# Kernel optimization log

Measured on AMD Instinct MI355X. Metric: run time of the kernel, lower is better.

## Reference

```python
import jax, jax.numpy as jnp
import numpy as np
import math

THETA = 2.0 ** 16  # rope theta from module (2**16)


def _freqs(n, theta):
    # get_freqs: quantize(arange(n), q=2) -> floor(i/2)*2; freqs = 1/theta**(q/n)/(2*pi)
    i = jnp.arange(n, dtype=jnp.float32)
    q = jnp.floor(i / 2.0) * 2.0
    return 1.0 / (theta ** (q / n)) / (2.0 * math.pi)


def _rope(phases, v):
    # interleaved rotation: v_rot = stack((-v[...,1::2], v[...,::2]), -1).reshape(v.shape)
    v_rot = jnp.stack((-v[..., 1::2], v[..., ::2]), axis=-1).reshape(v.shape)
    ph = (phases % 1.0) * (2.0 * math.pi)
    return v * jnp.cos(ph) + v_rot * jnp.sin(ph)


def setup_inputs() -> dict:
    key = jax.random.key(0)
    k1, k2, k3 = jax.random.split(key, 3)
    B, H, T, N = 2, 12, 2048, 256
    Q = jax.random.normal(k1, (B, H, T, N), dtype=jnp.float32)
    K = jax.random.normal(k2, (B, H, T, N), dtype=jnp.float32)
    V = jax.random.normal(k3, (B, H, T, N), dtype=jnp.float32)
    return {"Q": Q, "K": K, "V": V}


def reference(Q, K, V):
    T, N = Q.shape[2], Q.shape[3]
    freqs = _freqs(N, THETA)                                    # [N]
    phases = jnp.arange(T, dtype=jnp.float32)[:, None] * freqs  # [T, N]
    QR = _rope(phases, Q)
    KR = _rope(phases, K)
    # strictly-causal (diagonal=-1) non-softmax linear attention
    scores = jnp.einsum('bhtn,bhsn->bhts', QR, KR)
    scores = jnp.tril(scores, k=-1)
    return jnp.einsum('bhts,bhsn->bhtn', scores, V)
```

## Files before the change

### kernel.cpp

```cpp
#include <hip/hip_runtime.h>

typedef __bf16 bf16_t;
typedef short s16x8 __attribute__((ext_vector_type(8)));
typedef __bf16 bf16x4 __attribute__((ext_vector_type(4)));
typedef float f32x4 __attribute__((ext_vector_type(4)));

#define BH   24
#define TT   2048
#define NN   256

__global__ __launch_bounds__(256) void rope_qk_kernel(
    const float* __restrict__ Q, const float* __restrict__ K,
    bf16_t* __restrict__ QR, bf16_t* __restrict__ KR)
{
    int gid = blockIdx.x * 256 + threadIdx.x;
    int idx = gid * 8;
    int n0 = idx & (NN - 1);
    int t  = (idx >> 8) & (TT - 1);

    float4 q0 = *(const float4*)(Q + idx);
    float4 q1 = *(const float4*)(Q + idx + 4);
    float4 k0 = *(const float4*)(K + idx);
    float4 k1 = *(const float4*)(K + idx + 4);
    float qv[8] = {q0.x, q0.y, q0.z, q0.w, q1.x, q1.y, q1.z, q1.w};
    float kv[8] = {k0.x, k0.y, k0.z, k0.w, k1.x, k1.y, k1.z, k1.w};

    bf16_t qo[8], ko[8];
    #pragma unroll
    for (int j = 0; j < 4; j++) {
        int n = n0 + 2 * j;
        float freq = exp2f(-(float)n * 0.0625f) * 0.15915494309189535f;
        float ph = (float)t * freq;
        float r = ph - floorf(ph);
        float s = __builtin_amdgcn_sinf(r);
        float c = __builtin_amdgcn_cosf(r);
        qo[2*j]   = (bf16_t)(qv[2*j] * c - qv[2*j+1] * s);
        qo[2*j+1] = (bf16_t)(qv[2*j+1] * c + qv[2*j] * s);
        ko[2*j]   = (bf16_t)(kv[2*j] * c - kv[2*j+1] * s);
        ko[2*j+1] = (bf16_t)(kv[2*j+1] * c + kv[2*j] * s);
    }
    *(s16x8*)(QR + idx) = *(s16x8*)qo;
    *(s16x8*)(KR + idx) = *(s16x8*)ko;
}

__global__ __launch_bounds__(256) void vtrans_kernel(
    const float* __restrict__ V, bf16_t* __restrict__ Vt)
{
    __shared__ bf16_t tile[64][68];
    int bh = blockIdx.z;
    int t0 = blockIdx.x * 64;
    int n0 = blockIdx.y * 64;
    int rr = threadIdx.x >> 4;
    int c4 = (threadIdx.x & 15) * 4;

    const float* vb = V + ((long)bh * TT + t0) * NN + n0;
    #pragma unroll
    for (int i = 0; i < 4; i++) {
        int row = rr + i * 16;
        float4 v = *(const float4*)(vb + (long)row * NN + c4);
        bf16x4 b;
        b[0] = (bf16_t)v.x; b[1] = (bf16_t)v.y; b[2] = (bf16_t)v.z; b[3] = (bf16_t)v.w;
        *(bf16x4*)&tile[row][c4] = b;
    }
    __syncthreads();
    bf16_t* ob = Vt + ((long)bh * NN + n0) * TT + t0;
    #pragma unroll
    for (int i = 0; i < 4; i++) {
        int n = rr + i * 16;
        bf16x4 b;
        b[0] = tile[c4 + 0][n]; b[1] = tile[c4 + 1][n];
        b[2] = tile[c4 + 2][n]; b[3] = tile[c4 + 3][n];
        *(bf16x4*)(ob + (long)n * TT + c4) = b;
    }
}

__global__ __launch_bounds__(256, 2) void attn_kernel(
    const bf16_t* __restrict__ QR, const bf16_t* __restrict__ KR,
    const bf16_t* __restrict__ Vt, float* __restrict__ Out)
{
    __shared__ bf16_t kr_s[32][256];
    __shared__ bf16_t vt_s[256][40];
    __shared__ bf16_t s_s[4][32][40];

    int bh   = blockIdx.y;
    int qt   = 15 - (int)blockIdx.x;
    int t0   = qt * 128;
    int tid  = threadIdx.x;
    int wave = tid >> 6;
    int lane = tid & 63;
    int lrow = lane & 15;
    int lhi  = lane >> 4;
    int trow_base = t0 + wave * 32;

    s16x8 qfrag[2][8];
    #pragma unroll
    for (int rt = 0; rt < 2; rt++) {
        const bf16_t* qb = QR + ((long)bh * TT + trow_base + rt * 16 + lrow) * NN + lhi * 8;
        #pragma unroll
        for (int kb = 0; kb < 8; kb++)
            qfrag[rt][kb] = *(const s16x8*)(qb + kb * 32);
    }

    f32x4 zero4 = {0.0f, 0.0f, 0.0f, 0.0f};
    f32x4 oacc[2][16];
    #pragma unroll
    for (int rt = 0; rt < 2; rt++)
        #pragma unroll
        for (int nt = 0; nt < 16; nt++) oacc[rt][nt] = zero4;

    int krow  = tid >> 3;
    int kcolb = (tid & 7) * 64;
    const bf16_t* krbase = KR + ((long)bh * TT + krow) * NN + (tid & 7) * 32;
    const bf16_t* vtbase = Vt + ((long)bh * NN + tid) * TT;

    int ns = (t0 + 128) >> 5;
    for (int st = 0; st < ns; st++) {
        int s0 = st << 5;

        {
            const bf16_t* src = krbase + (long)s0 * NN;
            char* dst = (char*)(&kr_s[0][0]) + krow * 512;
            #pragma unroll
            for (int c = 0; c < 4; c++) {
                s16x8 v = *(const s16x8*)(src + c * 8);
                *(s16x8*)(dst + ((kcolb + c * 16) ^ ((krow & 7) << 4))) = v;
            }
        }
        {
            const bf16_t* src = vtbase + s0;
            #pragma unroll
            for (int c = 0; c < 4; c++)
                *(s16x8*)(&vt_s[tid][c * 8]) = *(const s16x8*)(src + c * 8);
        }
        __syncthreads();

        if (s0 < trow_base + 32) {
            f32x4 sacc[2][2];
            sacc[0][0] = zero4; sacc[0][1] = zero4; sacc[1][0] = zero4; sacc[1][1] = zero4;
            #pragma unroll
            for (int kb = 0; kb < 8; kb++) {
                #pragma unroll
                for (int h2 = 0; h2 < 2; h2++) {
                    int srow = h2 * 16 + lrow;
                    s16x8 bfr = *(const s16x8*)((char*)(&kr_s[0][0]) + srow * 512 +
                                    ((kb * 64 + lhi * 16) ^ ((srow & 7) << 4)));
                    sacc[0][h2] = __builtin_amdgcn_mfma_f32_16x16x32_bf16(
                                      qfrag[0][kb], bfr, sacc[0][h2], 0, 0, 0);
                    sacc[1][h2] = __builtin_amdgcn_mfma_f32_16x16x32_bf16(
                                      qfrag[1][kb], bfr, sacc[1][h2], 0, 0, 0);
                }
            }
            #pragma unroll
            for (int rt = 0; rt < 2; rt++)
                #pragma unroll
                for (int h2 = 0; h2 < 2; h2++)
                    #pragma unroll
                    for (int r = 0; r < 4; r++) {
                        int t_g = trow_base + rt * 16 + lhi * 4 + r;
                        int s_g = s0 + h2 * 16 + lrow;
                        float v = (s_g < t_g) ? sacc[rt][h2][r] : 0.0f;
                        s_s[wave][rt * 16 + lhi * 4 + r][h2 * 16 + lrow] = (bf16_t)v;
                    }
            s16x8 afr0 = *(const s16x8*)(&s_s[wave][lrow][lhi * 8]);
            s16x8 afr1 = *(const s16x8*)(&s_s[wave][16 + lrow][lhi * 8]);
            #pragma unroll
            for (int nt = 0; nt < 16; nt++) {
                s16x8 bfr = *(const s16x8*)(&vt_s[nt * 16 + lrow][lhi * 8]);
                oacc[0][nt] = __builtin_amdgcn_mfma_f32_16x16x32_bf16(afr0, bfr, oacc[0][nt], 0, 0, 0);
                oacc[1][nt] = __builtin_amdgcn_mfma_f32_16x16x32_bf16(afr1, bfr, oacc[1][nt], 0, 0, 0);
            }
        }
        __syncthreads();
    }

    #pragma unroll
    for (int rt = 0; rt < 2; rt++) {
        float* ob = Out + ((long)bh * TT + trow_base + rt * 16 + lhi * 4) * NN + lrow;
        #pragma unroll
        for (int nt = 0; nt < 16; nt++)
            #pragma unroll
            for (int r = 0; r < 4; r++)
                ob[(long)r * NN + nt * 16] = oacc[rt][nt][r];
    }
}

extern "C" void kernel_launch(void* const* d_in, const int* in_sizes, int n_in,
                              void* d_out, int out_size, void* d_ws, size_t ws_size,
                              hipStream_t stream) {
    const float* Q = (const float*)d_in[0];
    const float* K = (const float*)d_in[1];
    const float* V = (const float*)d_in[2];
    float* Out = (float*)d_out;

    const long TOT = (long)BH * TT * NN;
    bf16_t* qr = (bf16_t*)d_ws;
    bf16_t* kr = qr + TOT;
    bf16_t* vt = kr + TOT;

    rope_qk_kernel<<<dim3((int)(TOT / 8 / 256)), dim3(256), 0, stream>>>(Q, K, qr, kr);
    vtrans_kernel<<<dim3(TT / 64, NN / 64, BH), dim3(256), 0, stream>>>(V, vt);
    attn_kernel<<<dim3(TT / 128, BH), dim3(256), 0, stream>>>(qr, kr, vt, Out);
}
```

Measured before the change: 406.5 us.

## Split attention into 64-row tiles with split-K atomics for balanced causal work

```diff
diff --git a/kernel.cpp b/kernel.cpp
--- a/kernel.cpp
+++ b/kernel.cpp
@@ -8,6 +8,15 @@
 #define BH   24
 #define TT   2048
 #define NN   256
+
+__global__ __launch_bounds__(256) void zero_upper_kernel(float* __restrict__ Out)
+{
+    int gid = blockIdx.x * 256 + threadIdx.x;
+    int bh  = gid >> 16;
+    int off = gid & 65535;
+    float4* p = (float4*)(Out + (long)bh * (TT * NN) + 1024 * NN);
+    p[off] = make_float4(0.f, 0.f, 0.f, 0.f);
+}
 
 __global__ __launch_bounds__(256) void rope_qk_kernel(
     const float* __restrict__ Q, const float* __restrict__ K,
@@ -74,113 +83,122 @@
     }
 }
 
-__global__ __launch_bounds__(256, 2) void attn_kernel(
+__global__ __launch_bounds__(256, 3) void attn_kernel(
     const bf16_t* __restrict__ QR, const bf16_t* __restrict__ KR,
     const bf16_t* __restrict__ Vt, float* __restrict__ Out)
 {
-    __shared__ bf16_t kr_s[32][256];
+    __shared__ bf16_t kr_s[32 * 256];
     __shared__ bf16_t vt_s[256][40];
-    __shared__ bf16_t s_s[4][32][40];
-
-    int bh   = blockIdx.y;
-    int qt   = 15 - (int)blockIdx.x;
-    int t0   = qt * 128;
+    __shared__ bf16_t s_s[4][16][40];
+
+    int bh = blockIdx.y;
+    int x  = blockIdx.x;
+    int qt    = (x < 16) ? (16 + x) : (47 - x);
+    int chunk = (x >= 16 && x < 32) ? 1 : 0;
+    bool doAtomic = (qt >= 16);
+    int t0 = qt * 64;
+
     int tid  = threadIdx.x;
     int wave = tid >> 6;
     int lane = tid & 63;
     int lrow = lane & 15;
     int lhi  = lane >> 4;
-    int trow_base = t0 + wave * 32;
-
-    s16x8 qfrag[2][8];
-    #pragma unroll
-    for (int rt = 0; rt < 2; rt++) {
-        const bf16_t* qb = QR + ((long)bh * TT + trow_base + rt * 16 + lrow) * NN + lhi * 8;
+    int trow = t0 + wave * 16;
+
+    s16x8 qfrag[8];
+    {
+        const bf16_t* qb = QR + ((long)bh * TT + trow + lrow) * NN + lhi * 8;
         #pragma unroll
         for (int kb = 0; kb < 8; kb++)
-            qfrag[rt][kb] = *(const s16x8*)(qb + kb * 32);
-    }
-
-    f32x4 zero4 = {0.0f, 0.0f, 0.0f, 0.0f};
-    f32x4 oacc[2][16];
-    #pragma unroll
-    for (int rt = 0; rt < 2; rt++)
-        #pragma unroll
-        for (int nt = 0; nt < 16; nt++) oacc[rt][nt] = zero4;
-
-    int krow  = tid >> 3;
-    int kcolb = (tid & 7) * 64;
-    const bf16_t* krbase = KR + ((long)bh * TT + krow) * NN + (tid & 7) * 32;
-    const bf16_t* vtbase = Vt + ((long)bh * NN + tid) * TT;
-
-    int ns = (t0 + 128) >> 5;
-    for (int st = 0; st < ns; st++) {
+            qfrag[kb] = *(const s16x8*)(qb + kb * 32);
+    }
+
+    f32x4 zero4 = {0.f, 0.f, 0.f, 0.f};
+    f32x4 oacc[16];
+    #pragma unroll
+    for (int nt = 0; nt < 16; nt++) oacc[nt] = zero4;
+
+    int krow = tid >> 3;
+    int kch  = tid & 7;
+    const bf16_t* krsrc = KR + ((long)bh * TT + krow) * NN + kch * 32;
+    char* krdst = (char*)kr_s + krow * 512 + ((kch << 4) ^ ((krow & 7) << 4));
+    const bf16_t* vtsrc = Vt + ((long)bh * NN + tid) * TT;
+
+    int s_lo = chunk ? 1024 : 0;
+    int s_hi = chunk ? (t0 + 64) : min(t0 + 64, 1024);
+    int st0 = s_lo >> 5, st1 = s_hi >> 5;
+
+    for (int st = st0; st < st1; st++) {
         int s0 = st << 5;
 
         {
-            const bf16_t* src = krbase + (long)s0 * NN;
-            char* dst = (char*)(&kr_s[0][0]) + krow * 512;
-            #pragma unroll
-            for (int c = 0; c < 4; c++) {
-                s16x8 v = *(const s16x8*)(src + c * 8);
-                *(s16x8*)(dst + ((kcolb + c * 16) ^ ((krow & 7) << 4))) = v;
-            }
+            const bf16_t* src = krsrc + (long)s0 * NN;
+            #pragma unroll
+            for (int i = 0; i < 4; i++)
+                *(s16x8*)(krdst + i * 128) = *(const s16x8*)(src + i * 8);
         }
         {
-            const bf16_t* src = vtbase + s0;
+            const bf16_t* src = vtsrc + s0;
             #pragma unroll
             for (int c = 0; c < 4; c++)
                 *(s16x8*)(&vt_s[tid][c * 8]) = *(const s16x8*)(src + c * 8);
         }
         __syncthreads();
 
-        if (s0 < trow_base + 32) {
-            f32x4 sacc[2][2];
-            sacc[0][0] = zero4; sacc[0][1] = zero4; sacc[1][0] = zero4; sacc[1][1] = zero4;
+        if (s0 < trow + 16) {
+            f32x4 sacc[2];
+            sacc[0] = zero4; sacc[1] = zero4;
             #pragma unroll
             for (int kb = 0; kb < 8; kb++) {
                 #pragma unroll
                 for (int h2 = 0; h2 < 2; h2++) {
                     int srow = h2 * 16 + lrow;
-                    s16x8 bfr = *(const s16x8*)((char*)(&kr_s[0][0]) + srow * 512 +
-                                    ((kb * 64 + lhi * 16) ^ ((srow & 7) << 4)));
-                    sacc[0][h2] = __builtin_amdgcn_mfma_f32_16x16x32_bf16(
-                                      qfrag[0][kb], bfr, sacc[0][h2], 0, 0, 0);
-                    sacc[1][h2] = __builtin_amdgcn_mfma_f32_16x16x32_bf16(
-                                      qfrag[1][kb], bfr, sacc[1][h2], 0, 0, 0);
+                    s16x8 bfr = *(const s16x8*)((char*)kr_s + srow * 512 + lhi * 128 +
+                                    ((kb << 4) ^ ((srow & 7) << 4)));
+                    sacc[h2] = __builtin_amdgcn_mfma_f32_16x16x32_bf16(
+                                   qfrag[kb], bfr, sacc[h2], 0, 0, 0);
                 }
             }
-            #pragma unroll
-            for (int rt = 0; rt < 2; rt++)
+            if (s0 + 32 > trow) {
                 #pragma unroll
                 for (int h2 = 0; h2 < 2; h2++)
                     #pragma unroll
                     for (int r = 0; r < 4; r++) {
-                        int t_g = trow_base + rt * 16 + lhi * 4 + r;
+                        int t_g = trow + lhi * 4 + r;
                         int s_g = s0 + h2 * 16 + lrow;
-                        float v = (s_g < t_g) ? sacc[rt][h2][r] : 0.0f;
-                        s_s[wave][rt * 16 + lhi * 4 + r][h2 * 16 + lrow] = (bf16_t)v;
+                        float v = (s_g < t_g) ? sacc[h2][r] : 0.0f;
+                        s_s[wave][lhi * 4 + r][h2 * 16 + lrow] = (bf16_t)v;
                     }
-            s16x8 afr0 = *(const s16x8*)(&s_s[wave][lrow][lhi * 8]);
-            s16x8 afr1 = *(const s16x8*)(&s_s[wave][16 + lrow][lhi * 8]);
+            } else {
+                #pragma unroll
+                for (int h2 = 0; h2 < 2; h2++)
+                    #pragma unroll
+                    for (int r = 0; r < 4; r++)
+                        s_s[wave][lhi * 4 + r][h2 * 16 + lrow] = (bf16_t)sacc[h2][r];
+            }
+            s16x8 afr = *(const s16x8*)(&s_s[wave][lrow][lhi * 8]);
             #pragma unroll
             for (int nt = 0; nt < 16; nt++) {
                 s16x8 bfr = *(const s16x8*)(&vt_s[nt * 16 + lrow][lhi * 8]);
-                oacc[0][nt] = __builtin_amdgcn_mfma_f32_16x16x32_bf16(afr0, bfr, oacc[0][nt], 0, 0, 0);
-                oacc[1][nt] = __builtin_amdgcn_mfma_f32_16x16x32_bf16(afr1, bfr, oacc[1][nt], 0, 0, 0);
+                oacc[nt] = __builtin_amdgcn_mfma_f32_16x16x32_bf16(afr, bfr, oacc[nt], 0, 0, 0);
             }
         }
         __syncthreads();
     }
 
-    #pragma unroll
-    for (int rt = 0; rt < 2; rt++) {
-        float* ob = Out + ((long)bh * TT + trow_base + rt * 16 + lhi * 4) * NN + lrow;
+    float* ob = Out + ((long)bh * TT + trow + lhi * 4) * NN + lrow;
+    if (doAtomic) {
         #pragma unroll
         for (int nt = 0; nt < 16; nt++)
             #pragma unroll
             for (int r = 0; r < 4; r++)
-                ob[(long)r * NN + nt * 16] = oacc[rt][nt][r];
+                atomicAdd(&ob[(long)r * NN + nt * 16], oacc[nt][r]);
+    } else {
+        #pragma unroll
+        for (int nt = 0; nt < 16; nt++)
+            #pragma unroll
+            for (int r = 0; r < 4; r++)
+                ob[(long)r * NN + nt * 16] = oacc[nt][r];
     }
 }
 
@@ -197,7 +215,8 @@
     bf16_t* kr = qr + TOT;
     bf16_t* vt = kr + TOT;
 
+    zero_upper_kernel<<<dim3(BH * 256), dim3(256), 0, stream>>>(Out);
     rope_qk_kernel<<<dim3((int)(TOT / 8 / 256)), dim3(256), 0, stream>>>(Q, K, qr, kr);
     vtrans_kernel<<<dim3(TT / 64, NN / 64, BH), dim3(256), 0, stream>>>(V, vt);
-    attn_kernel<<<dim3(TT / 128, BH), dim3(256), 0, stream>>>(qr, kr, vt, Out);
-}
+    attn_kernel<<<dim3(48, BH), dim3(256), 0, stream>>>(qr, kr, vt, Out);
+}
```

Result: faster. 352.4 us (-13.3%).

## Switch causal attention to chunked linear-attention state formulation

Applied to the files above, without the earlier changes.

```diff
diff --git a/kernel.cpp b/kernel.cpp
--- a/kernel.cpp
+++ b/kernel.cpp
@@ -5,182 +5,229 @@
 typedef __bf16 bf16x4 __attribute__((ext_vector_type(4)));
 typedef float f32x4 __attribute__((ext_vector_type(4)));
 
-#define BH   24
-#define TT   2048
-#define NN   256
-
-__global__ __launch_bounds__(256) void rope_qk_kernel(
-    const float* __restrict__ Q, const float* __restrict__ K,
-    bf16_t* __restrict__ QR, bf16_t* __restrict__ KR)
-{
-    int gid = blockIdx.x * 256 + threadIdx.x;
-    int idx = gid * 8;
-    int n0 = idx & (NN - 1);
-    int t  = (idx >> 8) & (TT - 1);
-
-    float4 q0 = *(const float4*)(Q + idx);
-    float4 q1 = *(const float4*)(Q + idx + 4);
-    float4 k0 = *(const float4*)(K + idx);
-    float4 k1 = *(const float4*)(K + idx + 4);
-    float qv[8] = {q0.x, q0.y, q0.z, q0.w, q1.x, q1.y, q1.z, q1.w};
-    float kv[8] = {k0.x, k0.y, k0.z, k0.w, k1.x, k1.y, k1.z, k1.w};
-
-    bf16_t qo[8], ko[8];
-    #pragma unroll
-    for (int j = 0; j < 4; j++) {
-        int n = n0 + 2 * j;
-        float freq = exp2f(-(float)n * 0.0625f) * 0.15915494309189535f;
-        float ph = (float)t * freq;
-        float r = ph - floorf(ph);
-        float s = __builtin_amdgcn_sinf(r);
-        float c = __builtin_amdgcn_cosf(r);
-        qo[2*j]   = (bf16_t)(qv[2*j] * c - qv[2*j+1] * s);
-        qo[2*j+1] = (bf16_t)(qv[2*j+1] * c + qv[2*j] * s);
-        ko[2*j]   = (bf16_t)(kv[2*j] * c - kv[2*j+1] * s);
-        ko[2*j+1] = (bf16_t)(kv[2*j+1] * c + kv[2*j] * s);
-    }
-    *(s16x8*)(QR + idx) = *(s16x8*)qo;
-    *(s16x8*)(KR + idx) = *(s16x8*)ko;
-}
-
-__global__ __launch_bounds__(256) void vtrans_kernel(
-    const float* __restrict__ V, bf16_t* __restrict__ Vt)
+#define BH 24
+#define TT 2048
+#define NN 256
+
+__global__ __launch_bounds__(256) void rope_trans_kernel(
+    const float* __restrict__ src, bf16_t* __restrict__ dstRow,
+    bf16_t* __restrict__ dstT, int doRope)
 {
     __shared__ bf16_t tile[64][68];
-    int bh = blockIdx.z;
-    int t0 = blockIdx.x * 64;
-    int n0 = blockIdx.y * 64;
-    int rr = threadIdx.x >> 4;
-    int c4 = (threadIdx.x & 15) * 4;
-
-    const float* vb = V + ((long)bh * TT + t0) * NN + n0;
+    int bh = blockIdx.z, t0 = blockIdx.x * 64, n0 = blockIdx.y * 64;
+    int rr = threadIdx.x >> 4, c4 = (threadIdx.x & 15) * 4;
     #pragma unroll
     for (int i = 0; i < 4; i++) {
         int row = rr + i * 16;
-        float4 v = *(const float4*)(vb + (long)row * NN + c4);
+        int t = t0 + row;
+        float4 v = *(const float4*)(src + ((long)bh * TT + t) * NN + n0 + c4);
         bf16x4 b;
-        b[0] = (bf16_t)v.x; b[1] = (bf16_t)v.y; b[2] = (bf16_t)v.z; b[3] = (bf16_t)v.w;
+        if (doRope) {
+            float f0 = exp2f(-(float)(n0 + c4) * 0.0625f) * 0.15915494309189535f;
+            float f1 = exp2f(-(float)(n0 + c4 + 2) * 0.0625f) * 0.15915494309189535f;
+            float p0 = (float)t * f0; p0 -= floorf(p0);
+            float p1 = (float)t * f1; p1 -= floorf(p1);
+            float s0 = __builtin_amdgcn_sinf(p0), c0 = __builtin_amdgcn_cosf(p0);
+            float s1 = __builtin_amdgcn_sinf(p1), c1 = __builtin_amdgcn_cosf(p1);
+            b[0] = (bf16_t)(v.x * c0 - v.y * s0);
+            b[1] = (bf16_t)(v.y * c0 + v.x * s0);
+            b[2] = (bf16_t)(v.z * c1 - v.w * s1);
+            b[3] = (bf16_t)(v.w * c1 + v.z * s1);
+        } else {
+            b[0] = (bf16_t)v.x; b[1] = (bf16_t)v.y; b[2] = (bf16_t)v.z; b[3] = (bf16_t)v.w;
+        }
         *(bf16x4*)&tile[row][c4] = b;
-    }
-    __syncthreads();
-    bf16_t* ob = Vt + ((long)bh * NN + n0) * TT + t0;
-    #pragma unroll
-    for (int i = 0; i < 4; i++) {
-        int n = rr + i * 16;
-        bf16x4 b;
-        b[0] = tile[c4 + 0][n]; b[1] = tile[c4 + 1][n];
-        b[2] = tile[c4 + 2][n]; b[3] = tile[c4 + 3][n];
-        *(bf16x4*)(ob + (long)n * TT + c4) = b;
+        if (dstRow) *(bf16x4*)(dstRow + ((long)bh * TT + t) * NN + n0 + c4) = b;
+    }
+    if (dstT) {
+        __syncthreads();
+        #pragma unroll
+        for (int i = 0; i < 4; i++) {
+            int n = rr + i * 16;
+            bf16x4 b;
+            b[0] = tile[c4][n]; b[1] = tile[c4 + 1][n];
+            b[2] = tile[c4 + 2][n]; b[3] = tile[c4 + 3][n];
+            *(bf16x4*)(dstT + ((long)bh * NN + n0 + n) * TT + t0 + c4) = b;
+        }
     }
 }
 
 __global__ __launch_bounds__(256, 2) void attn_kernel(
     const bf16_t* __restrict__ QR, const bf16_t* __restrict__ KR,
-    const bf16_t* __restrict__ Vt, float* __restrict__ Out)
+    const bf16_t* __restrict__ KRt, const bf16_t* __restrict__ Vt,
+    float* __restrict__ Out)
 {
-    __shared__ bf16_t kr_s[32][256];
-    __shared__ bf16_t vt_s[256][40];
-    __shared__ bf16_t s_s[4][32][40];
-
-    int bh   = blockIdx.y;
-    int qt   = 15 - (int)blockIdx.x;
-    int t0   = qt * 128;
-    int tid  = threadIdx.x;
-    int wave = tid >> 6;
-    int lane = tid & 63;
-    int lrow = lane & 15;
-    int lhi  = lane >> 4;
-    int trow_base = t0 + wave * 32;
-
-    s16x8 qfrag[2][8];
+    __shared__ bf16_t kr_s[64 * 256];
+    __shared__ bf16_t S_lds[64 * 256];
+    __shared__ bf16_t s_s[4][16][72];
+
+    int bh = blockIdx.y;
+    int seg = blockIdx.x & 3;
+    int nt  = blockIdx.x >> 2;
+    int tid = threadIdx.x;
+    int w = tid >> 6, lane = tid & 63, lrow = lane & 15, lhi = lane >> 4;
+
+    const bf16_t* QRb  = QR  + (long)bh * TT * NN;
+    const bf16_t* KRb  = KR  + (long)bh * TT * NN;
+    const bf16_t* KRtb = KRt + (long)bh * NN * TT;
+    const bf16_t* Vtb  = Vt  + (long)bh * NN * TT;
+
+    f32x4 zero4 = {0.f, 0.f, 0.f, 0.f};
+    f32x4 sacc[4][4];
     #pragma unroll
-    for (int rt = 0; rt < 2; rt++) {
-        const bf16_t* qb = QR + ((long)bh * TT + trow_base + rt * 16 + lrow) * NN + lhi * 8;
-        #pragma unroll
-        for (int kb = 0; kb < 8; kb++)
-            qfrag[rt][kb] = *(const s16x8*)(qb + kb * 32);
-    }
-
-    f32x4 zero4 = {0.0f, 0.0f, 0.0f, 0.0f};
-    f32x4 oacc[2][16];
-    #pragma unroll
-    for (int rt = 0; rt < 2; rt++)
-        #pragma unroll
-        for (int nt = 0; nt < 16; nt++) oacc[rt][nt] = zero4;
-
-    int krow  = tid >> 3;
-    int kcolb = (tid & 7) * 64;
-    const bf16_t* krbase = KR + ((long)bh * TT + krow) * NN + (tid & 7) * 32;
-    const bf16_t* vtbase = Vt + ((long)bh * NN + tid) * TT;
-
-    int ns = (t0 + 128) >> 5;
-    for (int st = 0; st < ns; st++) {
-        int s0 = st << 5;
+    for (int i = 0; i < 4; i++)
+        #pragma unroll
+        for (int j = 0; j < 4; j++) sacc[i][j] = zero4;
+
+    const bf16_t* kabase = KRtb + ((long)(w * 64 + lrow)) * TT + lhi * 8;
+    const bf16_t* vbbase = Vtb  + ((long)(nt * 64 + lrow)) * TT + lhi * 8;
+
+    int send = seg * 512;
+    for (int s0 = 0; s0 < send; s0 += 128) {
+        s16x8 kaA[4][2], vbA[4][2], kaB[4][2], vbB[4][2];
+        #pragma unroll
+        for (int i = 0; i < 4; i++)
+            #pragma unroll
+            for (int k2 = 0; k2 < 2; k2++) {
+                kaA[i][k2] = *(const s16x8*)(kabase + (long)i * 16 * TT + s0 + k2 * 32);
+                kaB[i][k2] = *(const s16x8*)(kabase + (long)i * 16 * TT + s0 + 64 + k2 * 32);
+            }
+        #pragma unroll
+        for (int j = 0; j < 4; j++)
+            #pragma unroll
+            for (int k2 = 0; k2 < 2; k2++) {
+                vbA[j][k2] = *(const s16x8*)(vbbase + (long)j * 16 * TT + s0 + k2 * 32);
+                vbB[j][k2] = *(const s16x8*)(vbbase + (long)j * 16 * TT + s0 + 64 + k2 * 32);
+            }
+        #pragma unroll
+        for (int i = 0; i < 4; i++)
+            #pragma unroll
+            for (int j = 0; j < 4; j++)
+                #pragma unroll
+                for (int k2 = 0; k2 < 2; k2++) {
+                    sacc[i][j] = __builtin_amdgcn_mfma_f32_16x16x32_bf16(kaA[i][k2], vbA[j][k2], sacc[i][j], 0, 0, 0);
+                    sacc[i][j] = __builtin_amdgcn_mfma_f32_16x16x32_bf16(kaB[i][k2], vbB[j][k2], sacc[i][j], 0, 0, 0);
+                }
+    }
+
+    auto writeS = [&]() {
+        #pragma unroll
+        for (int j = 0; j < 4; j++) {
+            int rv = j * 16 + lrow;
+            char* rowp = (char*)S_lds + rv * 512;
+            int swz = (rv & 7) << 4;
+            #pragma unroll
+            for (int i = 0; i < 4; i++) {
+                bf16x4 b;
+                b[0] = (bf16_t)sacc[i][j][0]; b[1] = (bf16_t)sacc[i][j][1];
+                b[2] = (bf16_t)sacc[i][j][2]; b[3] = (bf16_t)sacc[i][j][3];
+                *(bf16x4*)(rowp + ((w * 128 + i * 32 + lhi * 8) ^ swz)) = b;
+            }
+        }
+    };
+    writeS();
+    __syncthreads();
+
+    int krow = tid >> 2, kcb = (tid & 3) * 16;
+    const bf16_t* qbase = QRb + ((long)(w * 16 + lrow)) * NN + lhi * 8;
+
+    for (int ch = 0; ch < 8; ch++) {
+        int t0 = seg * 512 + ch * 64;
 
         {
-            const bf16_t* src = krbase + (long)s0 * NN;
-            char* dst = (char*)(&kr_s[0][0]) + krow * 512;
-            #pragma unroll
-            for (int c = 0; c < 4; c++) {
-                s16x8 v = *(const s16x8*)(src + c * 8);
-                *(s16x8*)(dst + ((kcolb + c * 16) ^ ((krow & 7) << 4))) = v;
-            }
-        }
-        {
-            const bf16_t* src = vtbase + s0;
-            #pragma unroll
-            for (int c = 0; c < 4; c++)
-                *(s16x8*)(&vt_s[tid][c * 8]) = *(const s16x8*)(src + c * 8);
-        }
-        __syncthreads();
-
-        if (s0 < trow_base + 32) {
-            f32x4 sacc[2][2];
-            sacc[0][0] = zero4; sacc[0][1] = zero4; sacc[1][0] = zero4; sacc[1][1] = zero4;
+            const char* srow = (const char*)(KRb + (long)(t0 + krow) * NN);
+            char* drow = (char*)kr_s + krow * 512;
+            int swz = (krow & 7) << 4;
+            #pragma unroll
+            for (int c = 0; c < 8; c++) {
+                int cb = kcb + c * 64;
+                *(s16x8*)(drow + (cb ^ swz)) = *(const s16x8*)(srow + cb);
+            }
+        }
+        __syncthreads();
+
+        s16x8 qa[8];
+        const bf16_t* qp = qbase + (long)t0 * NN;
+        #pragma unroll
+        for (int kb = 0; kb < 8; kb++) qa[kb] = *(const s16x8*)(qp + kb * 32);
+        s16x8 vb[4][2], ka[4][2];
+        #pragma unroll
+        for (int j = 0; j < 4; j++)
+            #pragma unroll
+            for (int k2 = 0; k2 < 2; k2++)
+                vb[j][k2] = *(const s16x8*)(vbbase + (long)j * 16 * TT + t0 + k2 * 32);
+        #pragma unroll
+        for (int i = 0; i < 4; i++)
+            #pragma unroll
+            for (int k2 = 0; k2 < 2; k2++)
+                ka[i][k2] = *(const s16x8*)(kabase + (long)i * 16 * TT + t0 + k2 * 32);
+
+        f32x4 oacc[4];
+        #pragma unroll
+        for (int j = 0; j < 4; j++) oacc[j] = zero4;
+        #pragma unroll
+        for (int kb = 0; kb < 8; kb++) {
+            #pragma unroll
+            for (int j = 0; j < 4; j++) {
+                int rv = j * 16 + lrow;
+                s16x8 sb = *(const s16x8*)((const char*)S_lds + rv * 512 +
+                               ((kb * 64 + lhi * 16) ^ ((rv & 7) << 4)));
+                oacc[j] = __builtin_amdgcn_mfma_f32_16x16x32_bf16(qa[kb], sb, oacc[j], 0, 0, 0);
+            }
+        }
+        __syncthreads();
+
+        f32x4 pacc[4];
+        #pragma unroll
+        for (int h = 0; h < 4; h++) {
+            if (h > w) continue;
+            pacc[h] = zero4;
             #pragma unroll
             for (int kb = 0; kb < 8; kb++) {
+                int rs = h * 16 + lrow;
+                s16x8 kf = *(const s16x8*)((const char*)kr_s + rs * 512 +
+                               ((kb * 64 + lhi * 16) ^ ((rs & 7) << 4)));
+                pacc[h] = __builtin_amdgcn_mfma_f32_16x16x32_bf16(qa[kb], kf, pacc[h], 0, 0, 0);
+            }
+        }
+        #pragma unroll
+        for (int h = 0; h < 4; h++) {
+            if (h > w) continue;
+            #pragma unroll
+            for (int r = 0; r < 4; r++) {
+                float v = pacc[h][r];
+                if (h == w && lrow >= lhi * 4 + r) v = 0.0f;
+                s_s[w][lhi * 4 + r][h * 16 + lrow] = (bf16_t)v;
+            }
+        }
+        if (!(w & 1)) {
+            #pragma unroll
+            for (int r = 0; r < 4; r++) s_s[w][lhi * 4 + r][(w + 1) * 16 + lrow] = (bf16_t)0.0f;
+        }
+        int nkb2 = (w >> 1) + 1;
+        #pragma unroll
+        for (int k2 = 0; k2 < 2; k2++) {
+            if (k2 >= nkb2) continue;
+            s16x8 pa = *(const s16x8*)(&s_s[w][lrow][k2 * 32 + lhi * 8]);
+            #pragma unroll
+            for (int j = 0; j < 4; j++)
+                oacc[j] = __builtin_amdgcn_mfma_f32_16x16x32_bf16(pa, vb[j][k2], oacc[j], 0, 0, 0);
+        }
+        #pragma unroll
+        for (int i = 0; i < 4; i++)
+            #pragma unroll
+            for (int j = 0; j < 4; j++)
                 #pragma unroll
-                for (int h2 = 0; h2 < 2; h2++) {
-                    int srow = h2 * 16 + lrow;
-                    s16x8 bfr = *(const s16x8*)((char*)(&kr_s[0][0]) + srow * 512 +
-                                    ((kb * 64 + lhi * 16) ^ ((srow & 7) << 4)));
-                    sacc[0][h2] = __builtin_amdgcn_mfma_f32_16x16x32_bf16(
-                                      qfrag[0][kb], bfr, sacc[0][h2], 0, 0, 0);
-                    sacc[1][h2] = __builtin_amdgcn_mfma_f32_16x16x32_bf16(
-                                      qfrag[1][kb], bfr, sacc[1][h2], 0, 0, 0);
-                }
-            }
-            #pragma unroll
-            for (int rt = 0; rt < 2; rt++)
-                #pragma unroll
-                for (int h2 = 0; h2 < 2; h2++)
-                    #pragma unroll
-                    for (int r = 0; r < 4; r++) {
-                        int t_g = trow_base + rt * 16 + lhi * 4 + r;
-                        int s_g = s0 + h2 * 16 + lrow;
-                        float v = (s_g < t_g) ? sacc[rt][h2][r] : 0.0f;
-                        s_s[wave][rt * 16 + lhi * 4 + r][h2 * 16 + lrow] = (bf16_t)v;
-                    }
-            s16x8 afr0 = *(const s16x8*)(&s_s[wave][lrow][lhi * 8]);
-            s16x8 afr1 = *(const s16x8*)(&s_s[wave][16 + lrow][lhi * 8]);
-            #pragma unroll
-            for (int nt = 0; nt < 16; nt++) {
-                s16x8 bfr = *(const s16x8*)(&vt_s[nt * 16 + lrow][lhi * 8]);
-                oacc[0][nt] = __builtin_amdgcn_mfma_f32_16x16x32_bf16(afr0, bfr, oacc[0][nt], 0, 0, 0);
-                oacc[1][nt] = __builtin_amdgcn_mfma_f32_16x16x32_bf16(afr1, bfr, oacc[1][nt], 0, 0, 0);
-            }
-        }
-        __syncthreads();
-    }
-
-    #pragma unroll
-    for (int rt = 0; rt < 2; rt++) {
-        float* ob = Out + ((long)bh * TT + trow_base + rt * 16 + lhi * 4) * NN + lrow;
-        #pragma unroll
-        for (int nt = 0; nt < 16; nt++)
+                for (int k2 = 0; k2 < 2; k2++)
+                    sacc[i][j] = __builtin_amdgcn_mfma_f32_16x16x32_bf16(ka[i][k2], vb[j][k2], sacc[i][j], 0, 0, 0);
+        writeS();
+        float* ob = Out + (long)bh * TT * NN + (long)(t0 + w * 16 + lhi * 4) * NN + nt * 64 + lrow;
+        #pragma unroll
+        for (int j = 0; j < 4; j++)
             #pragma unroll
             for (int r = 0; r < 4; r++)
-                ob[(long)r * NN + nt * 16] = oacc[rt][nt][r];
+                ob[(long)r * NN + j * 16] = oacc[j][r];
+        __syncthreads();
     }
 }
 
@@ -193,11 +240,14 @@
     float* Out = (float*)d_out;
 
     const long TOT = (long)BH * TT * NN;
-    bf16_t* qr = (bf16_t*)d_ws;
-    bf16_t* kr = qr + TOT;
-    bf16_t* vt = kr + TOT;
-
-    rope_qk_kernel<<<dim3((int)(TOT / 8 / 256)), dim3(256), 0, stream>>>(Q, K, qr, kr);
-    vtrans_kernel<<<dim3(TT / 64, NN / 64, BH), dim3(256), 0, stream>>>(V, vt);
-    attn_kernel<<<dim3(TT / 128, BH), dim3(256), 0, stream>>>(qr, kr, vt, Out);
+    bf16_t* qr  = (bf16_t*)d_ws;
+    bf16_t* kr  = qr + TOT;
+    bf16_t* krt = kr + TOT;
+    bf16_t* vt  = krt + TOT;
+
+    dim3 tg(TT / 64, NN / 64, BH);
+    rope_trans_kernel<<<tg, dim3(256), 0, stream>>>(Q, qr, nullptr, 1);
+    rope_trans_kernel<<<tg, dim3(256), 0, stream>>>(K, kr, krt, 1);
+    rope_trans_kernel<<<tg, dim3(256), 0, stream>>>(V, nullptr, vt, 0);
+    attn_kernel<<<dim3(16, BH), dim3(256), 0, stream>>>(qr, kr, krt, vt, Out);
 }
```

Result: faster. 335.0 us (-17.6%).
